# Kernel tuning notes

Measured on AMD Instinct MI355X. Metric: run time of the kernel, lower is better.

## Reference

```python
import jax, jax.numpy as jnp
from jax import lax
import numpy as np

DT_RANK = 2   # ceil(d_model=32 / 16)
D_STATE = 16

def conv3d(x, w, b=None):
    y = lax.conv_general_dilated(x, w, (1, 1, 1), 'SAME',
        dimension_numbers=('NCDHW', 'OIDHW', 'NCDHW'))
    if b is not None:
        y = y + b[None, :, None, None, None]
    return y

def instnorm(x, eps=1e-5):
    mu = x.mean((2, 3, 4), keepdims=True)
    var = x.var((2, 3, 4), keepdims=True)
    return (x - mu) / jnp.sqrt(var + eps)

def lrelu(x, a=0.1):
    return jnp.where(x >= 0, x, a * x)

def selective_scan(u, delta, A, Bm, Cm, D, z):
    # u, delta, z: (B,L,d); A: (d,n); Bm, Cm: (B,L,n); D: (d,)
    dA = jnp.exp(jnp.einsum('bld,dn->bldn', delta, A))
    dBu = jnp.einsum('bld,bln,bld->bldn', delta, Bm, u)
    def step(h, inp):
        dA_t, dBu_t, C_t = inp
        h = dA_t * h + dBu_t
        y = jnp.einsum('bdn,bn->bd', h, C_t)
        return h, y
    h0 = jnp.zeros(u.shape[:1] + A.shape, u.dtype)
    _, ys = lax.scan(step, h0, (dA.transpose(1, 0, 2, 3), dBu.transpose(1, 0, 2, 3), Cm.transpose(1, 0, 2)))
    y = ys.transpose(1, 0, 2) + u * D
    return y * jax.nn.silu(z)

def mamba_branch(xc, z, conv_w, conv_b, xproj_w, dtproj_w, dtproj_b, A_log, D):
    # xc: (B,d_in,L) pre-activation; z: (B,L,d_in)
    d = xc.shape[1]
    xp = jnp.pad(xc, ((0, 0), (0, 0), (conv_w.shape[-1] - 1, 0)))  # causal depthwise conv1d
    xp = lax.conv_general_dilated(xp, conv_w[:, None, :], (1,), 'VALID',
        dimension_numbers=('NCH', 'OIH', 'NCH'), feature_group_count=d)
    xt = jax.nn.silu(xp + conv_b[None, :, None]).transpose(0, 2, 1)  # (B,L,d)
    x_dbl = xt @ xproj_w.T
    dt = x_dbl[..., :DT_RANK]
    Bm = x_dbl[..., DT_RANK:DT_RANK + D_STATE]
    Cm = x_dbl[..., DT_RANK + D_STATE:]
    delta = jax.nn.softplus(dt @ dtproj_w.T + dtproj_b)
    A = -jnp.exp(A_log)
    return selective_scan(xt, delta, A, Bm, Cm, D, z)

def reference(x, ln_g, ln_b, in_proj_w, conv1d_w, conv1d_bias, x_proj_w, dt_proj_w, dt_proj_bias, A_log, D_f, conv1db_w, conv1db_bias, x_projb_w, dt_projb_w, dt_projb_bias, Ab_log, D_b, out_proj_w, cp1_w, cp1_b, elk1_w, elk1_b, elk2_w, elk2_b, elk3_w, elk3_b, elk4_w, elk4_b, elk5_w, elk5_b, cp2_w, cp2_b, atten_w, conv1_w, conv2_w, conv2_b):
    B, C = x.shape[:2]
    img = x.shape[2:]
    L = img[0] * img[1] * img[2]
    x_conv, x_m = jnp.split(x, 2, axis=1)
    # --- Mamba branch (bimamba v2) ---
    xm = x_m.reshape(B, C // 2, L).transpose(0, 2, 1)  # (B,L,d_model)
    mu = xm.mean(-1, keepdims=True)
    var = xm.var(-1, keepdims=True)
    xm = (xm - mu) / jnp.sqrt(var + 1e-5) * ln_g + ln_b
    xz = xm @ in_proj_w.T  # (B,L,2*d_in)
    d_in = xz.shape[-1] // 2
    xi = xz[..., :d_in].transpose(0, 2, 1)  # (B,d_in,L)
    z = xz[..., d_in:]                       # (B,L,d_in)
    y_f = mamba_branch(xi, z, conv1d_w, conv1d_bias, x_proj_w, dt_proj_w, dt_proj_bias, A_log, D_f)
    y_b = mamba_branch(xi[:, :, ::-1], z[:, ::-1], conv1db_w, conv1db_bias, x_projb_w, dt_projb_w, dt_projb_bias, Ab_log, D_b)
    y = (y_f + y_b[:, ::-1]) @ out_proj_w.T  # (B,L,d_model)
    x_mamba = y.transpose(0, 2, 1).reshape(B, C // 2, *img)
    # --- conv path (ConvInsBlock -> ELK -> IN/LReLU -> ConvInsBlock) ---
    h = lrelu(instnorm(conv3d(x_conv, cp1_w, cp1_b)))
    e = jnp.concatenate([conv3d(h, elk1_w, elk1_b), conv3d(h, elk2_w, elk2_b),
                         conv3d(h, elk3_w, elk3_b), conv3d(h, elk4_w, elk4_b)], axis=1)
    h = conv3d(e, elk5_w, elk5_b) + h
    h = lrelu(instnorm(h))
    h = lrelu(instnorm(conv3d(h, cp2_w, cp2_b)))
    # --- fusion with channel shuffle + double-sigmoid channel attention ---
    xcat = jnp.concatenate([h, x_mamba], axis=1)
    fused = xcat.reshape(B, 2, C // 2, *img).transpose(0, 2, 1, 3, 4, 5).reshape(B, C, *img)
    pooled = fused.mean((2, 3, 4), keepdims=True)
    attn = jax.nn.sigmoid(jax.nn.sigmoid(conv3d(pooled, atten_w)))  # sigmoid applied twice, as in source
    fused = conv3d(fused * attn, conv1_w)
    attn2 = jax.nn.sigmoid(conv3d(xcat, conv2_w, conv2_b))
    return fused * attn2

def setup_inputs():
    ks = iter(jax.random.split(jax.random.key(0), 64))
    def nrm(shape, s=0.05):
        return jax.random.normal(next(ks), shape, jnp.float32) * s
    dim, div, d_in = 64, 32, 64
    A_init = jnp.tile(jnp.log(jnp.arange(1, D_STATE + 1, dtype=jnp.float32))[None, :], (d_in, 1))
    inp = {
        'x': jax.random.normal(next(ks), (1, dim, 32, 32, 16), jnp.float32),
        'ln_g': jnp.ones((div,), jnp.float32),
        'ln_b': jnp.zeros((div,), jnp.float32),
        'in_proj_w': nrm((2 * d_in, div)),
        'conv1d_w': nrm((d_in, 4), 0.2),
        'conv1d_bias': nrm((d_in,), 0.1),
        'x_proj_w': nrm((DT_RANK + 2 * D_STATE, d_in)),
        'dt_proj_w': nrm((d_in, DT_RANK), 0.5),
        'dt_proj_bias': jax.random.uniform(next(ks), (d_in,), jnp.float32, -4.0, -2.0),
        'A_log': A_init,
        'D_f': jnp.ones((d_in,), jnp.float32),
        'conv1db_w': nrm((d_in, 4), 0.2),
        'conv1db_bias': nrm((d_in,), 0.1),
        'x_projb_w': nrm((DT_RANK + 2 * D_STATE, d_in)),
        'dt_projb_w': nrm((d_in, DT_RANK), 0.5),
        'dt_projb_bias': jax.random.uniform(next(ks), (d_in,), jnp.float32, -4.0, -2.0),
        'Ab_log': A_init,
        'D_b': jnp.ones((d_in,), jnp.float32),
        'out_proj_w': nrm((div, d_in)),
        'cp1_w': nrm((div, div, 1, 1, 1)),
        'cp1_b': nrm((div,)),
        'elk1_w': nrm((div // 2, div, 3, 3, 3)),
        'elk1_b': nrm((div // 2,)),
        'elk2_w': nrm((div // 2, div, 5, 1, 1)),
        'elk2_b': nrm((div // 2,)),
        'elk3_w': nrm((div // 2, div, 1, 5, 1)),
        'elk3_b': nrm((div // 2,)),
        'elk4_w': nrm((div // 2, div, 1, 1, 5)),
        'elk4_b': nrm((div // 2,)),
        'elk5_w': nrm((div, 2 * div, 1, 1, 1)),
        'elk5_b': nrm((div,)),
        'cp2_w': nrm((div, div, 1, 1, 1)),
        'cp2_b': nrm((div,)),
        'atten_w': nrm((dim, dim, 1, 1, 1)),
        'conv1_w': nrm((dim, dim, 1, 1, 1)),
        'conv2_w': nrm((1, dim, 1, 1, 1)),
        'conv2_b': nrm((1,)),
    }
    return inp
```

## Files before the change

kernel.cpp:

```cpp
#include <hip/hip_runtime.h>
#include <math.h>

constexpr int L  = 16384;
constexpr int LC = 64;
constexpr int NC = 256;

constexpr int PX = 20, PY = 36, PZ = 36;
constexpr int PSY = PX;
constexpr int PSZ = PY*PX;
constexpr int PCH = PZ*PSZ;

__device__ __forceinline__ float sigm(float x){ return 1.0f/(1.0f+__expf(-x)); }
__device__ __forceinline__ float softplus_(float x){ return (x>20.0f)? x : log1pf(__expf(x)); }

__device__ __forceinline__ void block_accum2(float s, float s2, float* g0, float* g1){
    #pragma unroll
    for (int m=1;m<64;m<<=1){ s += __shfl_xor(s,m,64); s2 += __shfl_xor(s2,m,64); }
    __shared__ float red[16];
    int lane = threadIdx.x & 63, wid = threadIdx.x >> 6;
    if (lane==0){ red[wid]=s; red[8+wid]=s2; }
    __syncthreads();
    if (threadIdx.x==0){
        int nw = blockDim.x >> 6;
        float a=0.f,b=0.f;
        for (int i=0;i<nw;i++){ a+=red[i]; b+=red[8+i]; }
        atomicAdd(g0,a); atomicAdd(g1,b);
    }
}


__global__ __launch_bounds__(256,2)
void k_ln_proj(const float* __restrict__ x, const float* __restrict__ g,
               const float* __restrict__ b, const float* __restrict__ w,
               float* __restrict__ xi, float* __restrict__ z)
{
    __shared__ float xn[64][33];
    __shared__ float wt[32][36];
    int t  = threadIdx.x;
    int lq = t>>2, dc = t&3;
    int l  = blockIdx.x*64 + lq;
    int c0 = dc*8;
    int j0b = blockIdx.y*32;

    #pragma unroll
    for (int k=0;k<4;k++){
        int idx = t + k*256;
        int j = idx>>5, c = idx&31;
        wt[c][j] = w[(j0b+j)*32+c];
    }

    float xv[8]; float s=0.f, s2=0.f;
    #pragma unroll
    for (int cc=0;cc<8;cc++){
        float v = x[(32+c0+cc)*L + l];
        xv[cc]=v; s+=v; s2+=v*v;
    }
    #pragma unroll
    for (int m=1;m<4;m<<=1){ s += __shfl_xor(s,m,64); s2 += __shfl_xor(s2,m,64); }
    float mu  = s*(1.0f/32.0f);
    float var = s2*(1.0f/32.0f) - mu*mu;
    float inv = rsqrtf(var + 1e-5f);
    #pragma unroll
    for (int cc=0;cc<8;cc++)
        xn[lq][c0+cc] = (xv[cc]-mu)*inv*g[c0+cc] + b[c0+cc];
    __syncthreads();

    float acc[8];
    #pragma unroll
    for (int jj=0;jj<8;jj++) acc[jj]=0.f;
    #pragma unroll 4
    for (int c=0;c<32;c++){
        float uv = xn[lq][c];
        float4 w0 = *reinterpret_cast<const float4*>(&wt[c][dc*8]);
        float4 w1 = *reinterpret_cast<const float4*>(&wt[c][dc*8+4]);
        acc[0]+=w0.x*uv; acc[1]+=w0.y*uv; acc[2]+=w0.z*uv; acc[3]+=w0.w*uv;
        acc[4]+=w1.x*uv; acc[5]+=w1.y*uv; acc[6]+=w1.z*uv; acc[7]+=w1.w*uv;
    }
    int j0 = j0b + dc*8;
    if (j0 < 64){
        #pragma unroll
        for (int jj=0;jj<8;jj++) xi[(j0+jj)*L+l] = acc[jj];
    } else {
        #pragma unroll
        for (int q=0;q<2;q++)
            *reinterpret_cast<float4*>(z + l*64 + (j0-64) + q*4) =
                make_float4(acc[q*4], acc[q*4+1], acc[q*4+2], acc[q*4+3]);
    }
}

__global__ __launch_bounds__(256,2)
void k_conv_proj(const float* __restrict__ xi,
    const float* __restrict__ cwf, const float* __restrict__ cbf,
    const float* __restrict__ xwf, const float* __restrict__ dwf, const float* __restrict__ dbf,
    const float* __restrict__ cwb, const float* __restrict__ cbb,
    const float* __restrict__ xwb, const float* __restrict__ dwb, const float* __restrict__ dbb,
    float* __restrict__ uf, float* __restrict__ dlf, float* __restrict__ Bfp, float* __restrict__ Cfp,
    float* __restrict__ ub, float* __restrict__ dlb, float* __restrict__ Bbp, float* __restrict__ Cbp)
{
    __shared__ float uls[64][65];
    __shared__ float xwt[64][36];
    int t  = threadIdx.x;
    int lq = t>>2, dc = t&3;
    int l  = blockIdx.x*64 + lq;
    int d0 = dc*16;
    int gd = blockIdx.y;
    const float* cw = gd? cwb:cwf; const float* cb = gd? cbb:cbf;
    const float* xw = gd? xwb:xwf; const float* dw = gd? dwb:dwf; const float* db = gd? dbb:dbf;
    float* up = gd? ub:uf; float* dp = gd? dlb:dlf;
    float* Bp = gd? Bbp:Bfp; float* Cp = gd? Cbp:Cfp;

    #pragma unroll
    for (int k=0;k<9;k++){
        int idx = t + k*256;
        if (idx < 34*64){
            int r = idx>>6, c = idx&63;
            xwt[c][r] = xw[idx];
        }
    }

    float u16[16];
    #pragma unroll
    for (int dd=0; dd<16; dd++){
        int d = d0+dd;
        float s = cb[d];
        #pragma unroll
        for (int k=0;k<4;k++){
            int j = l-3+k;
            float v = 0.0f;
            if (j>=0) v = xi[d*L + (gd ? (L-1-j) : j)];
            s += cw[d*4+k]*v;
        }
        float u = s*sigm(s);
        u16[dd] = u;
        uls[lq][d] = u;
    }
    #pragma unroll
    for (int q=0;q<4;q++)
        *reinterpret_cast<float4*>(up + l*64 + d0 + q*4) =
            make_float4(u16[q*4], u16[q*4+1], u16[q*4+2], u16[q*4+3]);
    __syncthreads();

    float acc[8]; float t0=0.f, t1=0.f;
    #pragma unroll
    for (int jj=0;jj<8;jj++) acc[jj]=0.f;
    int rb = 2 + dc*8;
    #pragma unroll 4
    for (int c=0;c<64;c++){
        float uv = uls[lq][c];
        float2 d01 = *reinterpret_cast<const float2*>(&xwt[c][0]);
        t0 += d01.x*uv; t1 += d01.y*uv;
        float2 p0 = *reinterpret_cast<const float2*>(&xwt[c][rb]);
        float2 p1 = *reinterpret_cast<const float2*>(&xwt[c][rb+2]);
        float2 p2 = *reinterpret_cast<const float2*>(&xwt[c][rb+4]);
        float2 p3 = *reinterpret_cast<const float2*>(&xwt[c][rb+6]);
        acc[0]+=p0.x*uv; acc[1]+=p0.y*uv; acc[2]+=p1.x*uv; acc[3]+=p1.y*uv;
        acc[4]+=p2.x*uv; acc[5]+=p2.y*uv; acc[6]+=p3.x*uv; acc[7]+=p3.y*uv;
    }
    float* BC = (dc<2)? (Bp + l*16 + dc*8) : (Cp + l*16 + (dc-2)*8);
    *reinterpret_cast<float4*>(BC)   = make_float4(acc[0],acc[1],acc[2],acc[3]);
    *reinterpret_cast<float4*>(BC+4) = make_float4(acc[4],acc[5],acc[6],acc[7]);

    float dl16[16];
    #pragma unroll
    for (int dd=0; dd<16; dd++){
        int d = d0+dd;
        float tt = t0*dw[d*2] + t1*dw[d*2+1] + db[d];
        dl16[dd] = softplus_(tt);
    }
    #pragma unroll
    for (int q=0;q<4;q++)
        *reinterpret_cast<float4*>(dp + l*64 + d0 + q*4) =
            make_float4(dl16[q*4], dl16[q*4+1], dl16[q*4+2], dl16[q*4+3]);
}

__global__ void k_scan1(const float* __restrict__ dlf, const float* __restrict__ Bf, const float* __restrict__ ufp,
                        const float* __restrict__ dlb, const float* __restrict__ Bb, const float* __restrict__ ubp,
                        const float* __restrict__ Af, const float* __restrict__ Ab,
                        float* __restrict__ chA, float* __restrict__ chB)
{
    int tid = threadIdx.x;
    int c = blockIdx.x, gd = blockIdx.y;
    const float* dl = gd? dlb:dlf; const float* Bv = gd? Bb:Bf; const float* u = gd? ubp:ufp;
    float A = -__expf((gd? Ab:Af)[tid]);
    int d = tid>>4, n = tid&15;
    float h=0.f, p=1.f;
    int base = c*LC;
    #pragma unroll 4
    for (int i=0;i<LC;i++){
        int l = base+i;
        float dv = dl[l*64+d];
        float da = __expf(dv*A);
        float bu = dv * Bv[l*16+n] * u[l*64+d];
        h = da*h + bu;
        p *= da;
    }
    int o = (gd*NC + c)*1024 + tid;
    chA[o]=p; chB[o]=h;
}

__global__ void k_scan_agg(const float* __restrict__ chA, const float* __restrict__ chB,
                           float* __restrict__ hst)
{
    int tid = threadIdx.x; int gd = blockIdx.x;
    float h=0.f;
    #pragma unroll 8
    for (int c=0;c<NC;c++){
        int o = (gd*NC + c)*1024 + tid;
        hst[o]=h;
        h = chA[o]*h + chB[o];
    }
}

__global__ void k_scan2(const float* __restrict__ dlf, const float* __restrict__ Bf,
                        const float* __restrict__ Cf, const float* __restrict__ ufp,
                        const float* __restrict__ dlb, const float* __restrict__ Bb,
                        const float* __restrict__ Cb, const float* __restrict__ ubp,
                        const float* __restrict__ Af, const float* __restrict__ Ab,
                        const float* __restrict__ Dfp, const float* __restrict__ Dbp,
                        const float* __restrict__ hst,
                        float* __restrict__ yf, float* __restrict__ yb)
{
    int tid = threadIdx.x;
    int c = blockIdx.x, gd = blockIdx.y;
    const float* dl = gd? dlb:dlf; const float* Bv = gd? Bb:Bf;
    const float* Cv = gd? Cb:Cf;  const float* u  = gd? ubp:ufp;
    float A = -__expf((gd? Ab:Af)[tid]);
    int d = tid>>4, n = tid&15;
    float Dd = (gd? Dbp:Dfp)[d];
    float h = hst[(gd*NC + c)*1024 + tid];
    int base = c*LC;
    for (int i=0;i<LC;i++){
        int l = base+i;
        float dv = dl[l*64+d];
        float uu = u[l*64+d];
        float da = __expf(dv*A);
        h = da*h + dv * Bv[l*16+n] * uu;
        float t = h * Cv[l*16+n];
        t += __shfl_xor(t,1,16); t += __shfl_xor(t,2,16);
        t += __shfl_xor(t,4,16); t += __shfl_xor(t,8,16);
        if (n==0){
            float r = t + uu*Dd;
            if (gd) yb[(L-1-l)*64+d] = r;
            else    yf[l*64+d]       = r;
        }
    }
}

__global__ __launch_bounds__(256,2)
void k_combine(const float* __restrict__ yf, const float* __restrict__ yb,
               const float* __restrict__ z, const float* __restrict__ opw,
               float* __restrict__ xm)
{
    __shared__ float yls[64][65];
    __shared__ float ot[64][36];
    int t  = threadIdx.x;
    int lq = t>>2, dc = t&3;
    int l  = blockIdx.x*64 + lq;
    int d0 = dc*16;

    #pragma unroll
    for (int k=0;k<8;k++){
        int idx = t + k*256;
        int j = idx>>6, c = idx&63;
        ot[c][j] = opw[idx];
    }

    #pragma unroll
    for (int q=0;q<4;q++){
        float4 a = *reinterpret_cast<const float4*>(yf + l*64 + d0 + q*4);
        float4 bq= *reinterpret_cast<const float4*>(yb + l*64 + d0 + q*4);
        float4 zq= *reinterpret_cast<const float4*>(z  + l*64 + d0 + q*4);
        yls[lq][d0+q*4+0] = (a.x+bq.x)*(zq.x*sigm(zq.x));
        yls[lq][d0+q*4+1] = (a.y+bq.y)*(zq.y*sigm(zq.y));
        yls[lq][d0+q*4+2] = (a.z+bq.z)*(zq.z*sigm(zq.z));
        yls[lq][d0+q*4+3] = (a.w+bq.w)*(zq.w*sigm(zq.w));
    }
    __syncthreads();

    float acc[8];
    #pragma unroll
    for (int jj=0;jj<8;jj++) acc[jj]=0.f;
    #pragma unroll 4
    for (int c=0;c<64;c++){
        float uv = yls[lq][c];
        float4 w0 = *reinterpret_cast<const float4*>(&ot[c][dc*8]);
        float4 w1 = *reinterpret_cast<const float4*>(&ot[c][dc*8+4]);
        acc[0]+=w0.x*uv; acc[1]+=w0.y*uv; acc[2]+=w0.z*uv; acc[3]+=w0.w*uv;
        acc[4]+=w1.x*uv; acc[5]+=w1.y*uv; acc[6]+=w1.z*uv; acc[7]+=w1.w*uv;
    }
    #pragma unroll
    for (int jj=0;jj<8;jj++) xm[(dc*8+jj)*L+l] = acc[jj];
}


__global__ void k_conv1x1(const float* __restrict__ in, const float* __restrict__ w,
                          const float* __restrict__ b, float* __restrict__ out,
                          float* __restrict__ st)
{
    int oc = blockIdx.x; int l0 = blockIdx.y*(L/8);
    float s=0.f, s2=0.f;
    for (int l=l0+threadIdx.x; l<l0+L/8; l+=256){
        float acc = b[oc];
        #pragma unroll
        for (int ic=0;ic<32;ic++) acc += w[oc*32+ic]*in[ic*L+l];
        out[oc*L+l]=acc; s+=acc; s2+=acc*acc;
    }
    block_accum2(s,s2, st+oc, st+32+oc);
}

__global__ void k_norm(float* __restrict__ buf, const float* __restrict__ st)
{
    int oc = blockIdx.x; int l0 = blockIdx.y*(L/8);
    float mu  = st[oc]*(1.0f/(float)L);
    float var = st[32+oc]*(1.0f/(float)L) - mu*mu;
    float inv = rsqrtf(var + 1e-5f);
    for (int l=l0+threadIdx.x; l<l0+L/8; l+=256){
        float v = (buf[oc*L+l]-mu)*inv;
        buf[oc*L+l] = (v>=0.0f)? v : 0.1f*v;
    }
}

__global__ void k_norm_pad(float* __restrict__ buf, const float* __restrict__ st,
                           float* __restrict__ pad)
{
    int oc = blockIdx.x; int l0 = blockIdx.y*(L/8);
    float mu  = st[oc]*(1.0f/(float)L);
    float var = st[32+oc]*(1.0f/(float)L) - mu*mu;
    float inv = rsqrtf(var + 1e-5f);
    for (int l=l0+threadIdx.x; l<l0+L/8; l+=256){
        float v = (buf[oc*L+l]-mu)*inv;
        v = (v>=0.0f)? v : 0.1f*v;
        buf[oc*L+l] = v;
        int zx = l>>9, yy=(l>>4)&31, xx=l&15;
        pad[oc*PCH + (zx+2)*PSZ + (yy+2)*PSY + (xx+2)] = v;
    }
}

__global__ __launch_bounds__(256,2)
void k_elk(const float* __restrict__ hp,
           const float* __restrict__ w1, const float* __restrict__ b1,
           const float* __restrict__ w2, const float* __restrict__ b2,
           const float* __restrict__ w3, const float* __restrict__ b3,
           const float* __restrict__ w4, const float* __restrict__ b4,
           float* __restrict__ e)
{
    int l = blockIdx.x*256 + threadIdx.x;
    int oc0 = blockIdx.y*2;
    int zx = l>>9, yy=(l>>4)&31, xx=l&15;
    const float* base = hp + (zx+2)*PSZ + (yy+2)*PSY + (xx+2);
    float a1[2],a2[2],a3[2],a4[2];
    #pragma unroll
    for (int o=0;o<2;o++){ a1[o]=b1[oc0+o]; a2[o]=b2[oc0+o]; a3[o]=b3[oc0+o]; a4[o]=b4[oc0+o]; }

    for (int ic=0; ic<32; ic++){
        const float* hb = base + ic*PCH;
        float in3[27];
        #pragma unroll
        for (int dz=0;dz<3;dz++)
        #pragma unroll
        for (int dy=0;dy<3;dy++)
        #pragma unroll
        for (int dx=0;dx<3;dx++)
            in3[(dz*3+dy)*3+dx] = hb[(dz-1)*PSZ + (dy-1)*PSY + (dx-1)];
        float z5[5], y5[5], x5[5];
        #pragma unroll
        for (int t=0;t<5;t++){
            z5[t] = hb[(t-2)*PSZ];
            y5[t] = hb[(t-2)*PSY];
            x5[t] = hb[(t-2)];
        }
        #pragma unroll
        for (int o=0;o<2;o++){
            const float* wp1 = w1 + ((oc0+o)*32+ic)*27;
            float a = a1[o];
            #pragma unroll
            for (int t=0;t<27;t++) a += wp1[t]*in3[t];
            a1[o]=a;
            const float* wp2 = w2 + ((oc0+o)*32+ic)*5;
            const float* wp3 = w3 + ((oc0+o)*32+ic)*5;
            const float* wp4 = w4 + ((oc0+o)*32+ic)*5;
            float s2a=a2[o], s3a=a3[o], s4a=a4[o];
            #pragma unroll
            for (int t=0;t<5;t++){
                s2a += wp2[t]*z5[t];
                s3a += wp3[t]*y5[t];
                s4a += wp4[t]*x5[t];
            }
            a2[o]=s2a; a3[o]=s3a; a4[o]=s4a;
        }
    }
    #pragma unroll
    for (int o=0;o<2;o++){
        e[(oc0+o)*L+l]      = a1[o];
        e[(16+oc0+o)*L+l]   = a2[o];
        e[(32+oc0+o)*L+l]   = a3[o];
        e[(48+oc0+o)*L+l]   = a4[o];
    }
}

__global__ void k_elk5(const float* __restrict__ e, const float* __restrict__ hres,
                       const float* __restrict__ w, const float* __restrict__ b,
                       float* __restrict__ h2, float* __restrict__ st)
{
    int oc = blockIdx.x; int l0 = blockIdx.y*(L/8);
    float s=0.f, s2=0.f;
    for (int l=l0+threadIdx.x; l<l0+L/8; l+=256){
        float acc = b[oc];
        #pragma unroll
        for (int m=0;m<64;m++) acc += w[oc*64+m]*e[m*L+l];
        acc += hres[oc*L+l];
        h2[oc*L+l]=acc; s+=acc; s2+=acc*acc;
    }
    block_accum2(s,s2, st+oc, st+32+oc);
}


__global__ void k_pool(const float* __restrict__ h3, const float* __restrict__ xm,
                       float* __restrict__ pooled)
{
    int fc = blockIdx.x; int l0 = blockIdx.y*(L/8);
    const float* src = (fc&1) ? xm + (fc>>1)*L : h3 + (fc>>1)*L;
    float s=0.f;
    for (int l=l0+threadIdx.x; l<l0+L/8; l+=256) s += src[l];
    #pragma unroll
    for (int m=1;m<64;m<<=1) s += __shfl_xor(s,m,64);
    __shared__ float red[4];
    int lane = threadIdx.x&63, wid = threadIdx.x>>6;
    if (lane==0) red[wid]=s;
    __syncthreads();
    if (threadIdx.x==0) atomicAdd(pooled+fc, red[0]+red[1]+red[2]+red[3]);
}

__global__ void k_attn(const float* __restrict__ pooled, const float* __restrict__ aw,
                       float* __restrict__ attn)
{
    __shared__ float pl[64];
    int t = threadIdx.x;
    pl[t] = pooled[t]*(1.0f/(float)L);
    __syncthreads();
    float acc=0.f;
    #pragma unroll
    for (int c=0;c<64;c++) acc += aw[t*64+c]*pl[c];
    attn[t] = sigm(sigm(acc));
}

__global__ __launch_bounds__(256,2)
void k_final(const float* __restrict__ h3, const float* __restrict__ xm,
             const float* __restrict__ attn, const float* __restrict__ w1,
             const float* __restrict__ c2w, const float* __restrict__ c2b,
             float* __restrict__ out)
{
    int l = blockIdx.x*blockDim.x + threadIdx.x;
    int o0 = blockIdx.y*16;
    float acc[16];
    #pragma unroll
    for (int o=0;o<16;o++) acc[o]=0.f;
    float a2 = c2b[0];
    #pragma unroll
    for (int i=0;i<32;i++){
        float hv = h3[i*L+l];
        float xv = xm[i*L+l];
        a2 += c2w[i]*hv + c2w[32+i]*xv;
        float fh = hv*attn[2*i];
        float fx = xv*attn[2*i+1];
        #pragma unroll
        for (int o=0;o<16;o++)
            acc[o] += w1[(o0+o)*64 + 2*i]*fh + w1[(o0+o)*64 + 2*i+1]*fx;
    }
    float at2 = sigm(a2);
    #pragma unroll
    for (int o=0;o<16;o++) out[(o0+o)*L+l] = acc[o]*at2;
}


extern "C" void kernel_launch(void* const* d_in, const int* in_sizes, int n_in,
                              void* d_out, int out_size, void* d_ws, size_t ws_size,
                              hipStream_t stream)
{
    const float* x         = (const float*)d_in[0];
    const float* ln_g      = (const float*)d_in[1];
    const float* ln_b      = (const float*)d_in[2];
    const float* in_proj_w = (const float*)d_in[3];
    const float* conv1d_w  = (const float*)d_in[4];
    const float* conv1d_b  = (const float*)d_in[5];
    const float* x_proj_w  = (const float*)d_in[6];
    const float* dt_proj_w = (const float*)d_in[7];
    const float* dt_proj_b = (const float*)d_in[8];
    const float* A_log     = (const float*)d_in[9];
    const float* D_f       = (const float*)d_in[10];
    const float* conv1db_w = (const float*)d_in[11];
    const float* conv1db_b = (const float*)d_in[12];
    const float* x_projb_w = (const float*)d_in[13];
    const float* dt_projb_w= (const float*)d_in[14];
    const float* dt_projb_b= (const float*)d_in[15];
    const float* Ab_log    = (const float*)d_in[16];
    const float* D_b       = (const float*)d_in[17];
    const float* out_proj_w= (const float*)d_in[18];
    const float* cp1_w     = (const float*)d_in[19];
    const float* cp1_b     = (const float*)d_in[20];
    const float* elk1_w    = (const float*)d_in[21];
    const float* elk1_b    = (const float*)d_in[22];
    const float* elk2_w    = (const float*)d_in[23];
    const float* elk2_b    = (const float*)d_in[24];
    const float* elk3_w    = (const float*)d_in[25];
    const float* elk3_b    = (const float*)d_in[26];
    const float* elk4_w    = (const float*)d_in[27];
    const float* elk4_b    = (const float*)d_in[28];
    const float* elk5_w    = (const float*)d_in[29];
    const float* elk5_b    = (const float*)d_in[30];
    const float* cp2_w     = (const float*)d_in[31];
    const float* cp2_b     = (const float*)d_in[32];
    const float* atten_w   = (const float*)d_in[33];
    const float* conv1_w   = (const float*)d_in[34];
    const float* conv2_w   = (const float*)d_in[35];
    const float* conv2_b   = (const float*)d_in[36];

    float* ws = (float*)d_ws;
    float* XI  = ws + 0;
    float* Z   = ws + 1048576;
    float* UF  = ws + 2097152;
    float* UB  = ws + 3145728;
    float* DLF = ws + 4194304;
    float* DLB = ws + 5242880;
    float* BF  = ws + 6291456;
    float* CF  = ws + 6553600;
    float* BB  = ws + 6815744;
    float* CB  = ws + 7077888;
    float* CHA = ws + 7340032;
    float* CHB = ws + 7864320;
    float* HST = ws + 8388608;
    float* YF  = ws + 8912896;
    float* YB  = ws + 9961472;
    float* XM  = ws + 11010048;
    float* H1  = ws + 11534336;
    float* E4  = ws + 12058624;
    float* H2  = ws + 13107200;
    float* H3  = ws + 13631488;
    float* ST  = ws + 14155776;
    float* H1P = XI;

    hipMemsetAsync(ST, 0, 256*sizeof(float), stream);

    k_ln_proj<<<dim3(L/64,4), 256, 0, stream>>>(x, ln_g, ln_b, in_proj_w, XI, Z);
    k_conv_proj<<<dim3(L/64,2), 256, 0, stream>>>(XI,
        conv1d_w, conv1d_b, x_proj_w, dt_proj_w, dt_proj_b,
        conv1db_w, conv1db_b, x_projb_w, dt_projb_w, dt_projb_b,
        UF, DLF, BF, CF, UB, DLB, BB, CB);
    k_scan1<<<dim3(NC,2), 1024, 0, stream>>>(DLF, BF, UF, DLB, BB, UB, A_log, Ab_log, CHA, CHB);
    k_scan_agg<<<2, 1024, 0, stream>>>(CHA, CHB, HST);
    k_scan2<<<dim3(NC,2), 1024, 0, stream>>>(DLF, BF, CF, UF, DLB, BB, CB, UB,
                                             A_log, Ab_log, D_f, D_b, HST, YF, YB);
    k_combine<<<dim3(L/64), 256, 0, stream>>>(YF, YB, Z, out_proj_w, XM);

    k_conv1x1<<<dim3(32,8), 256, 0, stream>>>(x, cp1_w, cp1_b, H1, ST);
    hipMemsetAsync(H1P, 0, 32*PCH*sizeof(float), stream);
    k_norm_pad<<<dim3(32,8), 256, 0, stream>>>(H1, ST, H1P);
    k_elk<<<dim3(L/256,8), 256, 0, stream>>>(H1P, elk1_w, elk1_b, elk2_w, elk2_b,
                                             elk3_w, elk3_b, elk4_w, elk4_b, E4);
    k_elk5<<<dim3(32,8), 256, 0, stream>>>(E4, H1, elk5_w, elk5_b, H2, ST+64);
    k_norm<<<dim3(32,8), 256, 0, stream>>>(H2, ST+64);
    k_conv1x1<<<dim3(32,8), 256, 0, stream>>>(H2, cp2_w, cp2_b, H3, ST+128);
    k_norm<<<dim3(32,8), 256, 0, stream>>>(H3, ST+128);

    k_pool<<<dim3(64,8), 256, 0, stream>>>(H3, XM, ST+192);
    k_attn<<<1, 64, 0, stream>>>(ST+192, atten_w, ST+256);
    k_final<<<dim3(L/256,4), 256, 0, stream>>>(H3, XM, ST+256, conv1_w, conv2_w, conv2_b,
                                               (float*)d_out);
}
```

Measured before the change: 393.5 us.

## Stage ELK conv input halo tiles in double-buffered shared memory

Result: no change. 392.4 us (-0.3%).

```diff
diff --git a/kernel.cpp b/kernel.cpp
--- a/kernel.cpp
+++ b/kernel.cpp
@@ -344,49 +344,85 @@
            const float* __restrict__ w4, const float* __restrict__ b4,
            float* __restrict__ e)
 {
-    int l = blockIdx.x*256 + threadIdx.x;
+    __shared__ float tile[2][2000];
+    int t  = threadIdx.x;
+    int b  = blockIdx.x;
+    int z0 = b>>1, yh = (b&1)*16;
+    int ty = t>>4, tx = t&15;
+    int l  = z0*512 + (yh+ty)*16 + tx;
     int oc0 = blockIdx.y*2;
-    int zx = l>>9, yy=(l>>4)&31, xx=l&15;
-    const float* base = hp + (zx+2)*PSZ + (yy+2)*PSY + (xx+2);
+
+    const float* src0 = hp + z0*PSZ + yh*PSY;
+    int co = 800 + (ty+2)*20 + (tx+2);
+
     float a1[2],a2[2],a3[2],a4[2];
     #pragma unroll
     for (int o=0;o<2;o++){ a1[o]=b1[oc0+o]; a2[o]=b2[oc0+o]; a3[o]=b3[oc0+o]; a4[o]=b4[oc0+o]; }
 
+    #pragma unroll
+    for (int k=0;k<8;k++){
+        int idx = t + k*256;
+        if (idx < 2000){
+            int zz = idx/400;
+            tile[0][idx] = src0[zz*PSZ + (idx - zz*400)];
+        }
+    }
+    __syncthreads();
+
     for (int ic=0; ic<32; ic++){
-        const float* hb = base + ic*PCH;
-        float in3[27];
+        int cur = ic&1;
+        float r[8];
+        if (ic<31){
+            const float* srcn = src0 + (ic+1)*PCH;
+            #pragma unroll
+            for (int k=0;k<8;k++){
+                int idx = t + k*256;
+                int zz = idx/400;
+                r[k] = (idx<2000) ? srcn[zz*PSZ + (idx - zz*400)] : 0.0f;
+            }
+        }
+        const float* tl = tile[cur];
+        float v[27];
         #pragma unroll
         for (int dz=0;dz<3;dz++)
         #pragma unroll
         for (int dy=0;dy<3;dy++)
         #pragma unroll
         for (int dx=0;dx<3;dx++)
-            in3[(dz*3+dy)*3+dx] = hb[(dz-1)*PSZ + (dy-1)*PSY + (dx-1)];
+            v[(dz*3+dy)*3+dx] = tl[co + (dz-1)*400 + (dy-1)*20 + (dx-1)];
         float z5[5], y5[5], x5[5];
         #pragma unroll
-        for (int t=0;t<5;t++){
-            z5[t] = hb[(t-2)*PSZ];
-            y5[t] = hb[(t-2)*PSY];
-            x5[t] = hb[(t-2)];
+        for (int q=0;q<5;q++){
+            z5[q] = tl[co + (q-2)*400];
+            y5[q] = tl[co + (q-2)*20];
+            x5[q] = tl[co + (q-2)];
         }
         #pragma unroll
         for (int o=0;o<2;o++){
             const float* wp1 = w1 + ((oc0+o)*32+ic)*27;
             float a = a1[o];
             #pragma unroll
-            for (int t=0;t<27;t++) a += wp1[t]*in3[t];
+            for (int q=0;q<27;q++) a += wp1[q]*v[q];
             a1[o]=a;
             const float* wp2 = w2 + ((oc0+o)*32+ic)*5;
             const float* wp3 = w3 + ((oc0+o)*32+ic)*5;
             const float* wp4 = w4 + ((oc0+o)*32+ic)*5;
             float s2a=a2[o], s3a=a3[o], s4a=a4[o];
             #pragma unroll
-            for (int t=0;t<5;t++){
-                s2a += wp2[t]*z5[t];
-                s3a += wp3[t]*y5[t];
-                s4a += wp4[t]*x5[t];
+            for (int q=0;q<5;q++){
+                s2a += wp2[q]*z5[q];
+                s3a += wp3[q]*y5[q];
+                s4a += wp4[q]*x5[q];
             }
             a2[o]=s2a; a3[o]=s3a; a4[o]=s4a;
+        }
+        if (ic<31){
+            #pragma unroll
+            for (int k=0;k<8;k++){
+                int idx = t + k*256;
+                if (idx < 2000) tile[cur^1][idx] = r[k];
+            }
+            __syncthreads();
         }
     }
     #pragma unroll
```
